# Performance work log

Measured on AMD Instinct MI355X. Metric: run time of the kernel, lower is better.

Reference implementation:

```python
import jax, jax.numpy as jnp
import numpy as np

D1 = 3                     # lattice dimension (d == d1 == 3 in the original code)
S = 384                    # 2D grid size (s)
SCALE = S // 2 - 2         # coordinate scaling applied in get_model.forward

ELEVATE = jnp.asarray(np.array([[2, -1, -1], [-1, 2, -1], [-1, -1, 2]], np.float32) / np.sqrt(6.0).astype(np.float32))

def _canonical():
    c = np.tile(np.arange(D1), (D1, 1))
    for i in range(1, D1):
        c[-i:, i] = i - D1
    return jnp.asarray(c, jnp.int32)

CANONICAL = _canonical()   # (3, 3)


def setup_inputs() -> dict:
    key = jax.random.key(0)
    x = jax.random.normal(key, (64, 6, 8192), dtype=jnp.float32)
    return {"x": x}


def lattice_splat(pc, features):
    # pc: (B, 3, N) scaled coords; features: (B, c, N)
    B, _, N = pc.shape
    c = features.shape[1]

    elevated = jnp.einsum('ij,bjn->bin', ELEVATE, pc)        # (B,3,N)
    greedy = jnp.round(elevated / D1) * D1
    el_minus_gr = elevated - greedy

    # rank = inverse permutation of descending argsort along dim 1
    order = jnp.argsort(-el_minus_gr, axis=1)
    rank = jnp.argsort(order, axis=1)                        # (B,3,N) int

    remainder_sum = greedy.sum(axis=1, keepdims=True) / D1   # (B,1,N)
    rank_f = rank.astype(jnp.float32)
    cond = (((rank_f >= D1 - remainder_sum) & (remainder_sum > 0))
            | ((rank_f < -remainder_sum) & (remainder_sum < 0))).astype(jnp.float32)
    sign = jnp.where(remainder_sum > 0, -1.0, 0.0) + jnp.where(remainder_sum < 0, 1.0, 0.0)
    greedy = greedy + D1 * sign * cond
    rank = rank + (D1 * sign * cond).astype(rank.dtype) + remainder_sum.astype(rank.dtype)
    el_minus_gr = elevated - greedy
    greedy_i = greedy.astype(jnp.int32)

    # barycentric coordinates (faithful to original index arithmetic)
    b_idx = jnp.arange(B)[:, None, None]
    p_idx = jnp.arange(N)[None, None, :]
    bary = jnp.zeros((B, D1 + 1, N), jnp.float32)
    bary = bary.at[b_idx, 3 - rank, p_idx].add(el_minus_gr)
    bary = bary.at[b_idx, D1 - rank, p_idx].add(-el_minus_gr)
    bary = bary / D1
    bary = bary.at[:, 0, :].add(1.0 + bary[:, D1, :])
    bary = bary[:, :-1, :]                                   # (B,3,N)

    keys = greedy_i[:, :, :, None] + CANONICAL[rank]         # (B,3,N,3)

    # 2D coordinates from the first two key dims
    coord = keys[:, :2].reshape(B, 2, -1)                    # (B,2,3N)
    offset = coord.min(axis=2)                               # (B,2)
    coord = coord - offset[:, :, None]
    pts_pick = jnp.mod(-offset, D1)                          # (B,2)

    # splat values: barycentric-weighted features -> (B, 3N, c)
    tmp = bary[:, None, :, :] * features[:, :, None, :]      # (B,c,3,N)
    tmp = jnp.transpose(tmp, (0, 1, 3, 2)).reshape(B, c, -1) # (B,c,3N)
    tmp = jnp.transpose(tmp, (0, 2, 1))                      # (B,3N,c)

    # mask out-of-range lattice points
    out_any = (coord >= S).any(axis=1)                       # (B,3N)
    coord = jnp.where(coord >= S, 0, coord)
    tmp = jnp.where(out_any[:, :, None], 0.0, tmp)

    # sparse scatter-add into 2D grid (the kernel hotspot)
    splat = jnp.zeros((B, S, S, c), jnp.float32)
    bb = jnp.arange(B)[:, None]
    splat = splat.at[bb, coord[:, 0], coord[:, 1]].add(tmp)  # (B,S,S,c)

    # per-batch strided downsample with per-batch phase pts_pick
    g = S // D1
    rows = pts_pick[:, 0:1] + D1 * jnp.arange(g)[None, :]    # (B,g)
    cols = pts_pick[:, 1:2] + D1 * jnp.arange(g)[None, :]    # (B,g)
    f = jnp.take_along_axis(splat, rows[:, :, None, None], axis=1)  # (B,g,S,c)
    f = jnp.take_along_axis(f, cols[:, None, :, None], axis=2)      # (B,g,g,c)
    return f


def reference(x):
    features = x[:, 3:]                 # (B,3,N) normals as features
    pc = x[:, :3] * SCALE               # scaled xyz
    filt = lattice_splat(pc, features)  # (B, S//3, S//3, c)
    return jnp.transpose(filt, (0, 3, 1, 2))  # NCHW, input to the 2D backbone
```

## Files before the change

kernel.cpp:

```cpp
#include <hip/hip_runtime.h>

#define NB    64
#define NPT   8192
#define GSZ   128
#define TPB   1024
#define BPB   4
#define NBLK  (NB * BPB)
#define ROWS  32

typedef float vf4 __attribute__((ext_vector_type(4)));

__device__ __forceinline__ void compute_pt(float v0, float v1, float v2,
                                           int& u0o, int& u1o) {
    const float s6 = (float)2.449489742783178098197284074705891391989;
    const float ca = 2.0f / s6;
    const float cb = -1.0f / s6;
    const float y3 = 0.333333343267440796f;
    float p0 = v0 * 190.0f;
    float p1 = v1 * 190.0f;
    float p2 = v2 * 190.0f;
    float ev0 = __builtin_fmaf(cb, p2, __builtin_fmaf(cb, p1, ca * p0));
    float ev1 = __builtin_fmaf(cb, p2, __builtin_fmaf(ca, p1, cb * p0));
    float ev2 = __builtin_fmaf(ca, p2, __builtin_fmaf(cb, p1, cb * p0));
    float t0 = ev0 * y3, t1 = ev1 * y3, t2 = ev2 * y3;
    float q0 = __builtin_fmaf(__builtin_fmaf(-3.0f, t0, ev0), y3, t0);
    float q1 = __builtin_fmaf(__builtin_fmaf(-3.0f, t1, ev1), y3, t1);
    float q2 = __builtin_fmaf(__builtin_fmaf(-3.0f, t2, ev2), y3, t2);
    float rg0 = rintf(q0), rg1 = rintf(q1), rg2 = rintf(q2);
    int u0 = (int)rg0, u1 = (int)rg1, u2 = (int)rg2;
    float e0 = ev0 - rg0 * 3.0f;
    float e1 = ev1 - rg1 * 3.0f;
    float e2 = ev2 - rg2 * 3.0f;
    int rk0 = (int)(e1 > e0) + (int)(e2 > e0);
    int rk1 = (int)(e0 >= e1) + (int)(e2 > e1);
    int rs = u0 + u1 + u2;
    if (rs > 0) {
        if (rk0 >= 3 - rs) u0 -= 1;
        if (rk1 >= 3 - rs) u1 -= 1;
    } else if (rs < 0) {
        if (rk0 < -rs) u0 += 1;
        if (rk1 < -rs) u1 += 1;
    }
    u0o = u0; u1o = u1;
}

__global__ __launch_bounds__(TPB, 4) void kone(const float* __restrict__ x,
                                               float* __restrict__ out) {
    const int wg = blockIdx.x;
    const int bid = ((wg & 7) << 5) | (wg >> 3);
    const int b = bid >> 2, r = bid & 3;
    const int t = threadIdx.x;
    const int rlo = r * ROWS;

    const float* xb = x + (size_t)b * 6 * NPT;
    const int n0 = 4 * t, n1 = 4 * t + 4096;
    const float4 A0 = *(const float4*)(xb + n0);
    const float4 A1 = *(const float4*)(xb + NPT + n0);
    const float4 A2 = *(const float4*)(xb + 2 * NPT + n0);
    const float4 B0 = *(const float4*)(xb + n1);
    const float4 B1 = *(const float4*)(xb + NPT + n1);
    const float4 B2 = *(const float4*)(xb + 2 * NPT + n1);

    float* ob = out + (size_t)b * 3 * GSZ * GSZ + rlo * GSZ;
    const vf4 z4 = {0.f, 0.f, 0.f, 0.f};
#pragma unroll
    for (int c = 0; c < 3; ++c)
        __builtin_nontemporal_store(z4, &((vf4*)(ob + c * GSZ * GSZ))[t]);

    int pk[8];
    int m0 = 0x7fffffff, m1 = 0x7fffffff;
    {
        const float* f0 = (const float*)&A0;
        const float* f1 = (const float*)&A1;
        const float* f2 = (const float*)&A2;
#pragma unroll
        for (int e = 0; e < 4; ++e) {
            int u0, u1;
            compute_pt(f0[e], f1[e], f2[e], u0, u1);
            m0 = min(m0, u0); m1 = min(m1, u1);
            pk[e] = (u0 & 0xffff) | (u1 << 16);
        }
    }
    {
        const float* f0 = (const float*)&B0;
        const float* f1 = (const float*)&B1;
        const float* f2 = (const float*)&B2;
#pragma unroll
        for (int e = 0; e < 4; ++e) {
            int u0, u1;
            compute_pt(f0[e], f1[e], f2[e], u0, u1);
            m0 = min(m0, u0); m1 = min(m1, u1);
            pk[4 + e] = (u0 & 0xffff) | (u1 << 16);
        }
    }
    for (int o = 32; o; o >>= 1) {
        m0 = min(m0, __shfl_down(m0, o));
        m1 = min(m1, __shfl_down(m1, o));
    }

    __shared__ int red0[16], red1[16];
    if ((t & 63) == 0) { red0[t >> 6] = m0; red1[t >> 6] = m1; }
    __syncthreads();
    int off0 = red0[0], off1 = red1[0];
#pragma unroll
    for (int i = 1; i < TPB / 64; ++i) {
        off0 = min(off0, red0[i]);
        off1 = min(off1, red1[i]);
    }

#pragma unroll
    for (int k = 0; k < 8; ++k) {
        int p = pk[k];
        int u0 = (int)(short)(p & 0xffff);
        int u1 = p >> 16;
        int i = u0 - off0, j = u1 - off1;
        int il = i - rlo;
        if ((unsigned)il < ROWS && (unsigned)j < GSZ) {
            int n = 4 * t + (k >> 2) * 4096 + (k & 3);
            float* o = ob + (size_t)il * GSZ + j;
            atomicAdd(o + 0 * GSZ * GSZ, xb[3 * NPT + n]);
            atomicAdd(o + 1 * GSZ * GSZ, xb[4 * NPT + n]);
            atomicAdd(o + 2 * GSZ * GSZ, xb[5 * NPT + n]);
        }
    }
}

extern "C" void kernel_launch(void* const* d_in, const int* in_sizes, int n_in,
                              void* d_out, int out_size, void* d_ws, size_t ws_size,
                              hipStream_t stream) {
    const float* x = (const float*)d_in[0];
    float* out = (float*)d_out;
    kone<<<NBLK, TPB, 0, stream>>>(x, out);
}
```

Measured before the change: 13.43 us.

## Replace global atomic scatter with LDS compaction and per-thread gather accumulation

Each block first compacts the points that land in its 32-row slice into shared-memory arrays, using a shared counter. Every thread then scans the full compacted list and accumulates the entries that hit its own 4-column cell group in registers. Each thread writes its results once with plain vector stores, so the kernel no longer needs to zero the output and then apply global float atomics. The cost is an O(cnt) scan per thread and 16 KB of extra LDS per block, which may lower occupancy. If more than 1024 points land in a slice, the kernel falls back to the old atomic path.

```diff
diff --git a/kernel.cpp b/kernel.cpp
--- a/kernel.cpp
+++ b/kernel.cpp
@@ -7,8 +7,7 @@
 #define BPB   4
 #define NBLK  (NB * BPB)
 #define ROWS  32
-
-typedef float vf4 __attribute__((ext_vector_type(4)));
+#define CAP   1024
 
 __device__ __forceinline__ void compute_pt(float v0, float v1, float v2,
                                            int& u0o, int& u1o) {
@@ -52,6 +51,11 @@
     const int t = threadIdx.x;
     const int rlo = r * ROWS;
 
+    __shared__ int red0[16], red1[16];
+    __shared__ int s_cnt;
+    __shared__ int   s_ij[CAP];
+    __shared__ float s_f0[CAP], s_f1[CAP], s_f2[CAP];
+
     const float* xb = x + (size_t)b * 6 * NPT;
     const int n0 = 4 * t, n1 = 4 * t + 4096;
     const float4 A0 = *(const float4*)(xb + n0);
@@ -60,12 +64,6 @@
     const float4 B0 = *(const float4*)(xb + n1);
     const float4 B1 = *(const float4*)(xb + NPT + n1);
     const float4 B2 = *(const float4*)(xb + 2 * NPT + n1);
-
-    float* ob = out + (size_t)b * 3 * GSZ * GSZ + rlo * GSZ;
-    const vf4 z4 = {0.f, 0.f, 0.f, 0.f};
-#pragma unroll
-    for (int c = 0; c < 3; ++c)
-        __builtin_nontemporal_store(z4, &((vf4*)(ob + c * GSZ * GSZ))[t]);
 
     int pk[8];
     int m0 = 0x7fffffff, m1 = 0x7fffffff;
@@ -97,9 +95,8 @@
         m0 = min(m0, __shfl_down(m0, o));
         m1 = min(m1, __shfl_down(m1, o));
     }
-
-    __shared__ int red0[16], red1[16];
     if ((t & 63) == 0) { red0[t >> 6] = m0; red1[t >> 6] = m1; }
+    if (t == 0) s_cnt = 0;
     __syncthreads();
     int off0 = red0[0], off1 = red1[0];
 #pragma unroll
@@ -116,11 +113,58 @@
         int i = u0 - off0, j = u1 - off1;
         int il = i - rlo;
         if ((unsigned)il < ROWS && (unsigned)j < GSZ) {
-            int n = 4 * t + (k >> 2) * 4096 + (k & 3);
-            float* o = ob + (size_t)il * GSZ + j;
-            atomicAdd(o + 0 * GSZ * GSZ, xb[3 * NPT + n]);
-            atomicAdd(o + 1 * GSZ * GSZ, xb[4 * NPT + n]);
-            atomicAdd(o + 2 * GSZ * GSZ, xb[5 * NPT + n]);
+            int idx = atomicAdd(&s_cnt, 1);
+            if (idx < CAP) {
+                int n = 4 * t + (k >> 2) * 4096 + (k & 3);
+                s_ij[idx] = (il << 7) | j;
+                s_f0[idx] = xb[3 * NPT + n];
+                s_f1[idx] = xb[4 * NPT + n];
+                s_f2[idx] = xb[5 * NPT + n];
+            }
+        }
+    }
+    __syncthreads();
+    const int cnt = s_cnt;
+    float* ob = out + (size_t)b * 3 * GSZ * GSZ + rlo * GSZ;
+
+    if (cnt <= CAP) {
+        const int myil = t >> 5, j0 = (t & 31) << 2;
+        float4 v0 = make_float4(0.f, 0.f, 0.f, 0.f), v1 = v0, v2 = v0;
+        for (int e = 0; e < cnt; ++e) {
+            int ij = s_ij[e];
+            int il = ij >> 7;
+            unsigned dj = (unsigned)((ij & 127) - j0);
+            if (il == myil && dj < 4u) {
+                float* pv0 = (float*)&v0;
+                float* pv1 = (float*)&v1;
+                float* pv2 = (float*)&v2;
+                pv0[dj] += s_f0[e];
+                pv1[dj] += s_f1[e];
+                pv2[dj] += s_f2[e];
+            }
+        }
+        ((float4*)(ob + 0 * GSZ * GSZ))[t] = v0;
+        ((float4*)(ob + 1 * GSZ * GSZ))[t] = v1;
+        ((float4*)(ob + 2 * GSZ * GSZ))[t] = v2;
+    } else {
+        const float4 z4 = make_float4(0.f, 0.f, 0.f, 0.f);
+#pragma unroll
+        for (int c = 0; c < 3; ++c) ((float4*)(ob + c * GSZ * GSZ))[t] = z4;
+        __syncthreads();
+#pragma unroll
+        for (int k = 0; k < 8; ++k) {
+            int p = pk[k];
+            int u0 = (int)(short)(p & 0xffff);
+            int u1 = p >> 16;
+            int i = u0 - off0, j = u1 - off1;
+            int il = i - rlo;
+            if ((unsigned)il < ROWS && (unsigned)j < GSZ) {
+                int n = 4 * t + (k >> 2) * 4096 + (k & 3);
+                float* o = ob + (size_t)il * GSZ + j;
+                atomicAdd(o + 0 * GSZ * GSZ, xb[3 * NPT + n]);
+                atomicAdd(o + 1 * GSZ * GSZ, xb[4 * NPT + n]);
+                atomicAdd(o + 2 * GSZ * GSZ, xb[5 * NPT + n]);
+            }
         }
     }
 }
```

Result: slower. 25.50 us (+89.9%).
